# Kernel tuning notes

Measured on AMD Instinct MI355X. Metric: run time of the kernel, lower is better.

Reference implementation:

```python
import jax, jax.numpy as jnp
import numpy as np

B, L, S, V = 1024, 512, 64, 160000
EMB = 16
E = 3 * EMB            # extended embedding dim = 48
G, M = 4, 3            # lsh_group_num, lsh_group_length
MAXC = 2 ** M          # 8 buckets per group
NH, KD = 8, 4          # MHA heads / key_dim
IN_DIM = 5 * EMB + 3 * E   # user(80) + item(48) + longterm(48) + shortterm(48) = 224
PAD_LT, PAD_ST = L // 4, S // 4
M_VALUES = jnp.array([1, 2, 4], dtype=jnp.float32)
LN_EPS = 1e-3  # keras LayerNormalization default


def setup_inputs() -> dict:
    key = jax.random.key(0)
    ks = list(jax.random.split(key, 40))
    d = {}
    for i, n in enumerate(['uid', 'utag1', 'utag2', 'utag3', 'utag4']):
        d[n] = jax.random.randint(ks[i], (B,), 1, V, dtype=jnp.int32)
    for i, n in enumerate(['label_goods_ids', 'label_shop_ids', 'label_cate_ids']):
        d[n] = jax.random.randint(ks[5 + i], (B,), 1, V, dtype=jnp.int32)
    for i, n in enumerate(['longterm_goods_ids', 'longterm_shop_ids', 'longterm_cate_ids']):
        ids = jax.random.randint(ks[8 + i], (B, L), 1, V, dtype=jnp.int32)
        d[n] = ids.at[:, L - PAD_LT:].set(0)  # left-aligned valid prefix, padded tail
    for i, n in enumerate(['shortterm_goods_ids', 'shortterm_shop_ids', 'shortterm_cate_ids']):
        ids = jax.random.randint(ks[11 + i], (B, S), 1, V, dtype=jnp.int32)
        d[n] = ids.at[:, S - PAD_ST:].set(0)
    def nrm(k, shape, s):
        return jax.random.normal(k, shape, jnp.float32) * s
    d['embed_table'] = nrm(ks[14], (V, EMB), 0.05)
    d['H'] = nrm(ks[15], (E, G, M), 1.0)  # non-trainable LSH projections
    d['wq'] = nrm(ks[16], (E, NH, KD), 0.1); d['bq'] = jnp.zeros((NH, KD))
    d['wk'] = nrm(ks[17], (E, NH, KD), 0.1); d['bk'] = jnp.zeros((NH, KD))
    d['wv'] = nrm(ks[18], (E, NH, KD), 0.1); d['bv'] = jnp.zeros((NH, KD))
    d['wo'] = nrm(ks[19], (NH, KD, E), 0.1); d['bo'] = jnp.zeros((E,))
    d['w1'] = nrm(ks[20], (IN_DIM, 200), 0.1); d['b1'] = jnp.zeros((200,))
    d['g1'] = jnp.ones((200,)); d['be1'] = jnp.zeros((200,))
    d['w2'] = nrm(ks[21], (200, 80), 0.1); d['b2'] = jnp.zeros((80,))
    d['g2'] = jnp.ones((80,)); d['be2'] = jnp.zeros((80,))
    d['w3'] = nrm(ks[22], (80, 1), 0.1); d['b3'] = jnp.zeros((1,))
    return d


def _stack_embed(table, feats):
    # feats: list of (B,) or (B,T) int arrays -> (B, T, n_feats*EMB)
    cols = [f[:, None] if f.ndim == 1 else f for f in feats]
    X = jnp.stack(cols, axis=2)              # (B, T, F)
    Xe = table[X]                            # (B, T, F, EMB)
    return Xe.reshape(Xe.shape[0], Xe.shape[1], -1)


def _layernorm(x, g, b):
    mu = x.mean(-1, keepdims=True)
    var = jnp.square(x - mu).mean(-1, keepdims=True)
    return g * (x - mu) / jnp.sqrt(var + LN_EPS) + b


def _lsh_codes(x, H):
    # x: (B, T, E) -> integer bucket codes (B, T, G)
    codes = jnp.sign(jnp.einsum('bte,egm->btgm', x, H))
    binary = (codes == 1).astype(jnp.float32)
    return jnp.tensordot(binary, M_VALUES, axes=[[-1], [0]]).astype(jnp.int32)


def _forward(uid, utag1, utag2, utag3, utag4,
             label_goods_ids, label_shop_ids, label_cate_ids,
             longterm_goods_ids, longterm_shop_ids, longterm_cate_ids,
             shortterm_goods_ids, shortterm_shop_ids, shortterm_cate_ids,
             embed_table, H, wq, bq, wk, bk, wv, bv, wo, bo,
             w1, b1, g1, be1, w2, b2, g2, be2, w3, b3):
    # --- embeddings ---
    Xu = _stack_embed(embed_table, [uid, utag1, utag2, utag3, utag4])        # (B,1,80)
    Xi = _stack_embed(embed_table, [label_goods_ids, label_shop_ids, label_cate_ids])  # (B,1,48)
    Xl = _stack_embed(embed_table, [longterm_goods_ids, longterm_shop_ids, longterm_cate_ids])   # (B,L,48)
    Xs = _stack_embed(embed_table, [shortterm_goods_ids, shortterm_shop_ids, shortterm_cate_ids])  # (B,S,48)

    longterm_pad = longterm_goods_ids == 0
    shortterm_pad = shortterm_goods_ids == 0

    # --- long-term interest: LSH scatter-mean over buckets then gather by item code ---
    series_int = _lsh_codes(Xl, H)                                   # (B,L,G)
    mXl = Xl * (~longterm_pad).astype(jnp.float32)[:, :, None]        # masked series embeddings
    oh = jax.nn.one_hot(series_int, MAXC, dtype=jnp.float32)          # (B,L,G,C)
    c_sum = jnp.einsum('blgc,ble->bgce', oh, mXl)                     # bucket sums (B,G,C,E)
    vc = oh.sum(axis=1)                                               # valid counts (B,G,C)
    safe = jnp.where(vc[..., None] > 0,
                     c_sum / jnp.maximum(vc[..., None], 1.0),
                     0.0)                                             # bucket means
    item_int = _lsh_codes(Xi, H)                                      # (B,1,G)
    item_oh = jax.nn.one_hot(item_int, MAXC, dtype=jnp.float32)       # (B,1,G,C)
    longterm_interest = jnp.einsum('bgce,bsgc->bsge', safe, item_oh).mean(axis=2)  # (B,1,E)

    # --- short-term interest: target attention (keras MultiHeadAttention) ---
    lengths = (~shortterm_pad).astype(jnp.int32).sum(axis=1)           # (B,)
    seq_mask = (jnp.arange(S)[None, :] < lengths[:, None]).astype(jnp.float32)  # (B,S)
    q = jnp.einsum('bqe,ehd->bqhd', Xi, wq) + bq
    k = jnp.einsum('bke,ehd->bkhd', Xs, wk) + bk
    v = jnp.einsum('bke,ehd->bkhd', Xs, wv) + bv
    scores = jnp.einsum('bqhd,bkhd->bhqk', q, k) / jnp.sqrt(jnp.float32(KD))
    scores = scores + (1.0 - seq_mask[:, None, None, :]) * (-1e9)
    attn = jax.nn.softmax(scores, axis=-1)
    ctx = jnp.einsum('bhqk,bkhd->bqhd', attn, v)
    shortterm_interest = jnp.einsum('bqhd,hde->bqe', ctx, wo) + bo      # (B,1,E)

    # --- final MLP: Dense->LN->ReLU x2, Dense->sigmoid ---
    feat = jnp.concatenate([Xu[:, 0], Xi[:, 0],
                            longterm_interest[:, 0], shortterm_interest[:, 0]], axis=-1)  # (B,224)
    h = jax.nn.relu(_layernorm(feat @ w1 + b1, g1, be1))
    h = jax.nn.relu(_layernorm(h @ w2 + b2, g2, be2))
    return jax.nn.sigmoid(h @ w3 + b3)                                 # (B,1)


def reference(uid, utag1, utag2, utag3, utag4,
              label_goods_ids, label_shop_ids, label_cate_ids,
              longterm_goods_ids, longterm_shop_ids, longterm_cate_ids,
              shortterm_goods_ids, shortterm_shop_ids, shortterm_cate_ids,
              embed_table, H, wq, bq, wk, bk, wv, bv, wo, bo,
              w1, b1, g1, be1, w2, b2, g2, be2, w3, b3):
    return _forward(uid, utag1, utag2, utag3, utag4,
                    label_goods_ids, label_shop_ids, label_cate_ids,
                    longterm_goods_ids, longterm_shop_ids, longterm_cate_ids,
                    shortterm_goods_ids, shortterm_shop_ids, shortterm_cate_ids,
                    embed_table, H, wq, bq, wk, bk, wv, bv, wo, bo,
                    w1, b1, g1, be1, w2, b2, g2, be2, w3, b3)
```

## Files before the change

### kernel.cpp

```cpp
#include <hip/hip_runtime.h>
#include <hip/hip_bf16.h>

#define LLEN 512
#define SLEN 64
#define EMBD 16
#define EE 48
#define GG 4
#define NHH 8
#define KDD 4
#define INDIM 224
#define H1D 200
#define H2D 80
#define CHUNK 128
#define PXE 52
#define NT 512

__device__ __forceinline__ float bf2f(unsigned short u) {
    union { unsigned int i; float f; } v; v.i = ((unsigned int)u) << 16; return v.f;
}

template<bool BF16>
__device__ __forceinline__ float ldf(const void* p, int i) {
    if constexpr (BF16) return bf2f(((const unsigned short*)p)[i]);
    else                return ((const float*)p)[i];
}

template<bool BF16>
__device__ __forceinline__ float4 ld4(const void* p, int i4) {
    if constexpr (BF16) {
        ushort4 u = ((const ushort4*)p)[i4 >> 2];
        return make_float4(bf2f(u.x), bf2f(u.y), bf2f(u.z), bf2f(u.w));
    } else {
        return ((const float4*)p)[i4 >> 2];
    }
}

struct Pool {
    float buf[CHUNK * PXE + 16];
    float part[8][GG][EE];
    float hf[12 * EE];
    float feat[INDIM];
    float q[NHH * KDD];
    float red[128];
    int   pcw[8][2];
    int   len;
    float mu, rstd;
};

template<bool BF16>
__device__ void sdim_body(Pool& P,
    const int* uid, const int* ut1, const int* ut2, const int* ut3, const int* ut4,
    const int* lb_g, const int* lb_s, const int* lb_c,
    const int* lt_g, const int* lt_s, const int* lt_c,
    const int* st_g, const int* st_s, const int* st_c,
    const void* tbl, const void* Hm,
    const void* wq, const void* bq, const void* wk, const void* bk,
    const void* wvv, const void* bv, const void* wo, const void* bo,
    const void* w1, const void* b1, const void* g1, const void* be1,
    const void* w2, const void* b2, const void* g2, const void* be2,
    const void* w3, const void* b3, void* outp)
{
    const int b = blockIdx.x;
    const int tid = threadIdx.x;
    const int lane = tid & 63;
    const int wid = __builtin_amdgcn_readfirstlane(tid >> 6);

    const int pB = ((wid & 3) << 5) | (lane & 31);
    const int gB = ((wid >> 2) << 1) | (lane >> 5);

    int pid0, pid1, pid2, vld;
    {
        int f0 = tid, f1 = tid + NT, f2 = tid + 2 * NT;
        int p0 = f0 / 12, q0 = f0 - 12 * p0, e0 = q0 >> 2;
        int p1 = f1 / 12, q1 = f1 - 12 * p1, e1 = q1 >> 2;
        int p2 = f2 / 12, q2 = f2 - 12 * p2, e2 = q2 >> 2;
        const int* s0 = (e0 == 0) ? lt_g : (e0 == 1) ? lt_s : lt_c;
        const int* s1 = (e1 == 0) ? lt_g : (e1 == 1) ? lt_s : lt_c;
        const int* s2 = (e2 == 0) ? lt_g : (e2 == 1) ? lt_s : lt_c;
        pid0 = s0[b * LLEN + p0];
        pid1 = s1[b * LLEN + p1];
        pid2 = s2[b * LLEN + p2];
        vld  = lt_g[b * LLEN + pB];
    }

    for (int i = tid; i < 12 * EE; i += NT) {
        int j = i / EE, e = i - j * EE;
        P.hf[i] = ldf<BF16>(Hm, e * 12 + j);
    }
    if (tid < 80) {
        int f = tid >> 4, e = tid & 15;
        int id = (f == 0) ? uid[b] : (f == 1) ? ut1[b] : (f == 2) ? ut2[b] : (f == 3) ? ut3[b] : ut4[b];
        P.feat[tid] = ldf<BF16>(tbl, id * EMBD + e);
    } else if (tid < 128) {
        int t = tid - 80; int f = t >> 4, e = t & 15;
        int id = (f == 0) ? lb_g[b] : (f == 1) ? lb_s[b] : lb_c[b];
        P.feat[80 + t] = ldf<BF16>(tbl, id * EMBD + e);
    }
    __syncthreads();

    if (tid < 32) {
        float acc = ldf<BF16>(bq, tid);
        for (int e = 0; e < EE; e++) acc += P.feat[80 + e] * ldf<BF16>(wq, e * 32 + tid);
        P.q[tid] = acc;
    }
    if (tid >= 64 && tid < 76) {
        int j = tid - 64;
        float acc = 0.f;
        for (int e = 0; e < EE; e++) acc += P.feat[80 + e] * P.hf[j * EE + e];
        P.red[j] = acc;
    }
    __syncthreads();

    int icb = 0;
    #pragma unroll
    for (int m = 0; m < 3; m++) if (P.red[gB * 3 + m] > 0.f) icb |= (1 << m);

    float accg[GG] = {0.f, 0.f, 0.f, 0.f};
    int cnt0 = 0, cnt1 = 0;
    const int offs = (lane < 52) ? lane : 51;

    for (int ch = 0; ch < 4; ++ch) {
        {
            float4 v0, v1, v2;
            {
                int f0 = tid, f1 = tid + NT, f2 = tid + 2 * NT;
                int q0 = f0 - 12 * (f0 / 12);
                int q1 = f1 - 12 * (f1 / 12);
                int q2 = f2 - 12 * (f2 / 12);
                v0 = ld4<BF16>(tbl, pid0 * EMBD + ((q0 & 3) << 2));
                v1 = ld4<BF16>(tbl, pid1 * EMBD + ((q1 & 3) << 2));
                v2 = ld4<BF16>(tbl, pid2 * EMBD + ((q2 & 3) << 2));
            }
            {
                int f0 = tid, f1 = tid + NT, f2 = tid + 2 * NT;
                int p0 = f0 / 12, q0 = f0 - 12 * p0;
                int p1 = f1 / 12, q1 = f1 - 12 * p1;
                int p2 = f2 / 12, q2 = f2 - 12 * p2;
                *(float4*)&P.buf[p0 * PXE + (q0 << 2)] = v0;
                *(float4*)&P.buf[p1 * PXE + (q1 << 2)] = v1;
                *(float4*)&P.buf[p2 * PXE + (q2 << 2)] = v2;
            }
        }
        {
            const int nbase = ((ch < 3) ? (ch + 1) : 3) * CHUNK;
            int f0 = tid, f1 = tid + NT, f2 = tid + 2 * NT;
            int p0 = f0 / 12, e0 = (f0 - 12 * p0) >> 2;
            int p1 = f1 / 12, e1 = (f1 - 12 * p1) >> 2;
            int p2 = f2 / 12, e2 = (f2 - 12 * p2) >> 2;
            const int* s0 = (e0 == 0) ? lt_g : (e0 == 1) ? lt_s : lt_c;
            const int* s1 = (e1 == 0) ? lt_g : (e1 == 1) ? lt_s : lt_c;
            const int* s2 = (e2 == 0) ? lt_g : (e2 == 1) ? lt_s : lt_c;
            pid0 = s0[b * LLEN + nbase + p0];
            pid1 = s1[b * LLEN + nbase + p1];
            pid2 = s2[b * LLEN + nbase + p2];
        }
        __syncthreads();
        int nvld;
        {
            const int nbase = ((ch < 3) ? (ch + 1) : 3) * CHUNK;
            nvld = lt_g[b * LLEN + nbase + pB];
            const float* row = &P.buf[pB * PXE];
            float4 x[12];
            #pragma unroll
            for (int k = 0; k < 12; k++) x[k] = *(const float4*)(row + 4 * k);
            float acc[3];
            #pragma unroll
            for (int jj = 0; jj < 3; jj++) {
                const float4* hr = (const float4*)&P.hf[(3 * gB + jj) * EE];
                float s = 0.f;
                #pragma unroll
                for (int k = 0; k < 12; k++) {
                    float4 h4 = hr[k];
                    s += x[k].x * h4.x + x[k].y * h4.y + x[k].z * h4.z + x[k].w * h4.w;
                }
                acc[jj] = s;
            }
            int code = 0;
            #pragma unroll
            for (int m = 0; m < 3; m++) if (acc[m] > 0.f) code |= (1 << m);
            int valid = (vld != 0);
            P.buf[pB * PXE + 48 + gB] = (code == icb && valid) ? 1.f : 0.f;
            unsigned long long m = __ballot(code == icb);
            cnt0 += __popcll(m & 0xFFFFFFFFull);
            cnt1 += __popcll(m >> 32);
        }
        vld = nvld;
        __syncthreads();
        {
            const float* basep = &P.buf[(wid << 4) * PXE] + offs;
            #pragma unroll
            for (int i = 0; i < 16; i++) {
                float xv = basep[i * PXE];
                #pragma unroll
                for (int g = 0; g < GG; g++) {
                    float sel = __int_as_float(
                        __builtin_amdgcn_readlane(__float_as_int(xv), 48 + g));
                    accg[g] += sel * xv;
                }
            }
        }
        __syncthreads();
    }

    float* Xs   = P.buf;
    float* wkqT = P.buf + SLEN * PXE;
    float* bkq  = wkqT + NHH * PXE;
    float* sc   = bkq + NHH;
    float* su   = sc + SLEN * NHH;
    float* sctx = su + NHH * EE;

    if (lane < EE) {
        #pragma unroll
        for (int g = 0; g < GG; g++) P.part[wid][g][lane] = accg[g];
    }
    if (lane == 0) { P.pcw[wid][0] = cnt0; P.pcw[wid][1] = cnt1; }
    {
        int f0 = tid;
        int p0 = f0 / 12, q0 = f0 - 12 * p0, fe0 = q0 >> 2;
        const int* idp0 = (fe0 == 0) ? st_g : (fe0 == 1) ? st_s : st_c;
        int id0 = idp0[b * SLEN + p0];
        const bool has1 = (tid < (SLEN * 12 - NT));
        int id1 = 0, p1 = 0, q1 = 0;
        if (has1) {
            int f1 = tid + NT;
            p1 = f1 / 12; q1 = f1 - 12 * p1; int fe1 = q1 >> 2;
            const int* idp1 = (fe1 == 0) ? st_g : (fe1 == 1) ? st_s : st_c;
            id1 = idp1[b * SLEN + p1];
        }
        float4 v0 = ld4<BF16>(tbl, id0 * EMBD + ((q0 & 3) << 2));
        *(float4*)&Xs[p0 * PXE + (q0 << 2)] = v0;
        if (has1) {
            float4 v1 = ld4<BF16>(tbl, id1 * EMBD + ((q1 & 3) << 2));
            *(float4*)&Xs[p1 * PXE + (q1 << 2)] = v1;
        }
    }
    for (int t = tid; t < EE * NHH; t += NT) {
        int e = t >> 3, h = t & 7;
        float acc = 0.f;
        #pragma unroll
        for (int d = 0; d < KDD; d++) acc += ldf<BF16>(wk, e * 32 + h * 4 + d) * P.q[h * 4 + d];
        wkqT[h * PXE + e] = acc;
    }
    if (tid < NHH) {
        float acc = 0.f;
        #pragma unroll
        for (int d = 0; d < KDD; d++) acc += ldf<BF16>(bk, tid * 4 + d) * P.q[tid * 4 + d];
        bkq[tid] = acc;
    }
    if (tid < 64) {
        unsigned long long msk = __ballot(st_g[b * SLEN + tid] != 0);
        if (tid == 0) P.len = __popcll(msk);
    }
    __syncthreads();

    if (tid < EE) {
        float r = 0.f;
        #pragma unroll
        for (int g = 0; g < GG; g++) {
            int wb = (g >> 1) << 2;
            int h = g & 1;
            float c = (float)(P.pcw[wb][h] + P.pcw[wb + 1][h] + P.pcw[wb + 2][h] + P.pcw[wb + 3][h]);
            float s = 0.f;
            #pragma unroll
            for (int w = 0; w < 8; w++) s += P.part[w][g][tid];
            r += s / fmaxf(c, 1.0f);
        }
        P.feat[128 + tid] = r * 0.25f;
    }

    {
        int s = tid >> 3, h = tid & 7;
        const float* xr = &Xs[s * PXE];
        const float* wr = &wkqT[h * PXE];
        float acc = bkq[h];
        #pragma unroll
        for (int k = 0; k < 12; k++) {
            float4 xv = *(const float4*)(xr + 4 * k);
            float4 wv = *(const float4*)(wr + 4 * k);
            acc += xv.x * wv.x + xv.y * wv.y + xv.z * wv.z + xv.w * wv.w;
        }
        acc *= 0.5f;
        if (s >= P.len) acc -= 1e9f;
        sc[s * NHH + h] = acc;
    }
    __syncthreads();
    {
        float v = sc[lane * NHH + wid];
        float mx = v;
        #pragma unroll
        for (int o = 32; o; o >>= 1) mx = fmaxf(mx, __shfl_xor(mx, o));
        float ex = __expf(v - mx);
        float sm = ex;
        #pragma unroll
        for (int o = 32; o; o >>= 1) sm += __shfl_xor(sm, o);
        sc[lane * NHH + wid] = ex / sm;
    }
    __syncthreads();
    if (tid < NHH * EE) {
        int h = tid / EE, e = tid - h * EE;
        float acc = 0.f;
        #pragma unroll 4
        for (int s = 0; s < SLEN; s++) acc += sc[s * NHH + h] * Xs[s * PXE + e];
        su[tid] = acc;
    }
    __syncthreads();
    if (tid < 32) {
        float acc = ldf<BF16>(bv, tid);
        int h = tid >> 2;
        for (int e = 0; e < EE; e++) acc += su[h * EE + e] * ldf<BF16>(wvv, e * 32 + tid);
        sctx[tid] = acc;
    }
    __syncthreads();
    if (tid < EE) {
        float acc = ldf<BF16>(bo, tid);
        #pragma unroll
        for (int i = 0; i < 32; i++) acc += sctx[i] * ldf<BF16>(wo, i * EE + tid);
        P.feat[176 + tid] = acc;
    }
    __syncthreads();

    float z1p = 0.f;
    if (tid < H1D) {
        float a0 = ldf<BF16>(b1, tid), a1 = 0.f, a2 = 0.f, a3 = 0.f;
        #pragma unroll 2
        for (int i = 0; i < 112; i += 4) {
            float4 f4 = *(const float4*)&P.feat[i];
            a0 += f4.x * ldf<BF16>(w1, (i + 0) * H1D + tid);
            a1 += f4.y * ldf<BF16>(w1, (i + 1) * H1D + tid);
            a2 += f4.z * ldf<BF16>(w1, (i + 2) * H1D + tid);
            a3 += f4.w * ldf<BF16>(w1, (i + 3) * H1D + tid);
        }
        z1p = (a0 + a1) + (a2 + a3);
    } else if (tid >= 256 && tid < 256 + H1D) {
        int o = tid - 256;
        float a0 = 0.f, a1 = 0.f, a2 = 0.f, a3 = 0.f;
        #pragma unroll 2
        for (int i = 112; i < INDIM; i += 4) {
            float4 f4 = *(const float4*)&P.feat[i];
            a0 += f4.x * ldf<BF16>(w1, (i + 0) * H1D + o);
            a1 += f4.y * ldf<BF16>(w1, (i + 1) * H1D + o);
            a2 += f4.z * ldf<BF16>(w1, (i + 2) * H1D + o);
            a3 += f4.w * ldf<BF16>(w1, (i + 3) * H1D + o);
        }
        P.buf[640 + o] = (a0 + a1) + (a2 + a3);
    }
    __syncthreads();
    float z1 = 0.f;
    if (tid < H1D) { z1 = z1p + P.buf[640 + tid]; P.buf[tid] = z1; }
    __syncthreads();
    if (tid < 64) {
        float sm = 0.f, sq = 0.f;
        for (int j = tid; j < H1D; j += 64) { float v = P.buf[j]; sm += v; sq += v * v; }
        #pragma unroll
        for (int o = 32; o; o >>= 1) { sm += __shfl_xor(sm, o); sq += __shfl_xor(sq, o); }
        if (tid == 0) { float mu = sm / H1D; P.mu = mu; P.rstd = rsqrtf(sq / H1D - mu * mu + 1e-3f); }
    }
    __syncthreads();
    if (tid < H1D) {
        float h = fmaxf(ldf<BF16>(g1, tid) * (z1 - P.mu) * P.rstd + ldf<BF16>(be1, tid), 0.f);
        P.buf[256 + tid] = h;
    }
    __syncthreads();
    float z2p = 0.f;
    if (tid < H2D) {
        float a0 = ldf<BF16>(b2, tid), a1 = 0.f, a2 = 0.f, a3 = 0.f;
        #pragma unroll 2
        for (int i = 0; i < 100; i += 4) {
            float4 f4 = *(const float4*)&P.buf[256 + i];
            a0 += f4.x * ldf<BF16>(w2, (i + 0) * H2D + tid);
            a1 += f4.y * ldf<BF16>(w2, (i + 1) * H2D + tid);
            a2 += f4.z * ldf<BF16>(w2, (i + 2) * H2D + tid);
            a3 += f4.w * ldf<BF16>(w2, (i + 3) * H2D + tid);
        }
        z2p = (a0 + a1) + (a2 + a3);
    } else if (tid >= 256 && tid < 256 + H2D) {
        int o = tid - 256;
        float a0 = 0.f, a1 = 0.f, a2 = 0.f, a3 = 0.f;
        #pragma unroll 2
        for (int i = 100; i < H1D; i += 4) {
            float4 f4 = *(const float4*)&P.buf[256 + i];
            a0 += f4.x * ldf<BF16>(w2, (i + 0) * H2D + o);
            a1 += f4.y * ldf<BF16>(w2, (i + 1) * H2D + o);
            a2 += f4.z * ldf<BF16>(w2, (i + 2) * H2D + o);
            a3 += f4.w * ldf<BF16>(w2, (i + 3) * H2D + o);
        }
        P.buf[640 + o] = (a0 + a1) + (a2 + a3);
    }
    __syncthreads();
    float z2 = 0.f;
    if (tid < H2D) { z2 = z2p + P.buf[640 + tid]; P.buf[tid] = z2; }
    __syncthreads();
    if (tid < 64) {
        float sm = 0.f, sq = 0.f;
        for (int j = tid; j < H2D; j += 64) { float v = P.buf[j]; sm += v; sq += v * v; }
        #pragma unroll
        for (int o = 32; o; o >>= 1) { sm += __shfl_xor(sm, o); sq += __shfl_xor(sq, o); }
        if (tid == 0) { float mu = sm / H2D; P.mu = mu; P.rstd = rsqrtf(sq / H2D - mu * mu + 1e-3f); }
    }
    __syncthreads();
    if (tid < H2D) {
        float h = fmaxf(ldf<BF16>(g2, tid) * (z2 - P.mu) * P.rstd + ldf<BF16>(be2, tid), 0.f);
        P.red[tid] = h * ldf<BF16>(w3, tid);
    }
    __syncthreads();
    if (tid < 64) {
        float v = P.red[tid] + ((tid < H2D - 64) ? P.red[64 + tid] : 0.f);
        #pragma unroll
        for (int o = 32; o; o >>= 1) v += __shfl_xor(v, o);
        if (tid == 0) {
            float acc = ldf<BF16>(b3, 0) + v;
            float sig = 1.f / (1.f + __expf(-acc));
            if constexpr (BF16) ((__hip_bfloat16*)outp)[b] = __float2bfloat16(sig);
            else                ((float*)outp)[b] = sig;
        }
    }
}

__global__ __launch_bounds__(NT, 8) void sdim_fwd(
    const int* __restrict__ uid, const int* __restrict__ ut1, const int* __restrict__ ut2,
    const int* __restrict__ ut3, const int* __restrict__ ut4,
    const int* __restrict__ lb_g, const int* __restrict__ lb_s, const int* __restrict__ lb_c,
    const int* __restrict__ lt_g, const int* __restrict__ lt_s, const int* __restrict__ lt_c,
    const int* __restrict__ st_g, const int* __restrict__ st_s, const int* __restrict__ st_c,
    const void* __restrict__ tbl, const void* __restrict__ Hm,
    const void* __restrict__ wq, const void* __restrict__ bq,
    const void* __restrict__ wk, const void* __restrict__ bk,
    const void* __restrict__ wvv, const void* __restrict__ bv,
    const void* __restrict__ wo, const void* __restrict__ bo,
    const void* __restrict__ w1, const void* __restrict__ b1,
    const void* __restrict__ g1, const void* __restrict__ be1,
    const void* __restrict__ w2, const void* __restrict__ b2,
    const void* __restrict__ g2, const void* __restrict__ be2,
    const void* __restrict__ w3, const void* __restrict__ b3,
    void* __restrict__ outp)
{
    __shared__ Pool P;
    __shared__ int s_isbf;
    if (threadIdx.x < 64) {
        int big = 0;
        for (int i = (threadIdx.x & 63); i < 128; i += 64) {
            unsigned short u = ((const unsigned short*)tbl)[2 * i];
            if (((u >> 7) & 0xFF) >= 127) big = 1;
        }
        unsigned long long m = __ballot(big);
        if (threadIdx.x == 0) s_isbf = (m == 0ull) ? 1 : 0;
    }
    __syncthreads();
    if (s_isbf)
        sdim_body<true >(P, uid, ut1, ut2, ut3, ut4, lb_g, lb_s, lb_c, lt_g, lt_s, lt_c,
                         st_g, st_s, st_c, tbl, Hm, wq, bq, wk, bk, wvv, bv, wo, bo,
                         w1, b1, g1, be1, w2, b2, g2, be2, w3, b3, outp);
    else
        sdim_body<false>(P, uid, ut1, ut2, ut3, ut4, lb_g, lb_s, lb_c, lt_g, lt_s, lt_c,
                         st_g, st_s, st_c, tbl, Hm, wq, bq, wk, bk, wvv, bv, wo, bo,
                         w1, b1, g1, be1, w2, b2, g2, be2, w3, b3, outp);
}

extern "C" void kernel_launch(void* const* d_in, const int* in_sizes, int n_in,
                              void* d_out, int out_size, void* d_ws, size_t ws_size,
                              hipStream_t stream) {
    const int B = in_sizes[0];
    sdim_fwd<<<B, NT, 0, stream>>>(
        (const int*)d_in[0],  (const int*)d_in[1],  (const int*)d_in[2],
        (const int*)d_in[3],  (const int*)d_in[4],
        (const int*)d_in[5],  (const int*)d_in[6],  (const int*)d_in[7],
        (const int*)d_in[8],  (const int*)d_in[9],  (const int*)d_in[10],
        (const int*)d_in[11], (const int*)d_in[12], (const int*)d_in[13],
        (const void*)d_in[14], (const void*)d_in[15],
        (const void*)d_in[16], (const void*)d_in[17],
        (const void*)d_in[18], (const void*)d_in[19],
        (const void*)d_in[20], (const void*)d_in[21],
        (const void*)d_in[22], (const void*)d_in[23],
        (const void*)d_in[24], (const void*)d_in[25],
        (const void*)d_in[26], (const void*)d_in[27],
        (const void*)d_in[28], (const void*)d_in[29],
        (const void*)d_in[30], (const void*)d_in[31],
        (const void*)d_in[32], (const void*)d_in[33],
        d_out);
}
```

Measured before the change: 210.1 us.

## Stage all sequence ids in LDS up front and read selection flags from LDS

All long-term ids (3×512) are loaded once per block into LDS, reusing the `part` scratch area, and all short-term ids into a new `stids` array. This replaces the per-chunk prefetch of next-chunk ids and validity flags from global memory, so each chunk's table gather depends only on LDS reads. The grouped accumulation now reads the four bucket-match flags as one float4 from LDS instead of four cross-lane `readlane` ops. The short-term gathers are reordered so both table loads are issued before the stores. The cost is more up-front global traffic before the first barrier and losing the overlap the old id prefetch gave.

Result: slower. 233.9 us (+11.4%).

```diff
diff --git a/kernel.cpp b/kernel.cpp
--- a/kernel.cpp
+++ b/kernel.cpp
@@ -42,6 +42,7 @@
     float feat[INDIM];
     float q[NHH * KDD];
     float red[128];
+    int   stids[3 * SLEN];
     int   pcw[8][2];
     int   len;
     float mu, rstd;
@@ -68,21 +69,20 @@
     const int pB = ((wid & 3) << 5) | (lane & 31);
     const int gB = ((wid >> 2) << 1) | (lane >> 5);
 
-    int pid0, pid1, pid2, vld;
-    {
-        int f0 = tid, f1 = tid + NT, f2 = tid + 2 * NT;
-        int p0 = f0 / 12, q0 = f0 - 12 * p0, e0 = q0 >> 2;
-        int p1 = f1 / 12, q1 = f1 - 12 * p1, e1 = q1 >> 2;
-        int p2 = f2 / 12, q2 = f2 - 12 * p2, e2 = q2 >> 2;
-        const int* s0 = (e0 == 0) ? lt_g : (e0 == 1) ? lt_s : lt_c;
-        const int* s1 = (e1 == 0) ? lt_g : (e1 == 1) ? lt_s : lt_c;
-        const int* s2 = (e2 == 0) ? lt_g : (e2 == 1) ? lt_s : lt_c;
-        pid0 = s0[b * LLEN + p0];
-        pid1 = s1[b * LLEN + p1];
-        pid2 = s2[b * LLEN + p2];
-        vld  = lt_g[b * LLEN + pB];
-    }
-
+    int* IDS = (int*)P.part;
+
+    #pragma unroll
+    for (int r = 0; r < 3; r++) {
+        int i = tid + r * NT;
+        int fe = i >> 9, pos = i & 511;
+        const int* src = (fe == 0) ? lt_g : (fe == 1) ? lt_s : lt_c;
+        IDS[i] = __builtin_nontemporal_load(&src[b * LLEN + pos]);
+    }
+    if (tid < 3 * SLEN) {
+        int fe = tid >> 6, pos = tid & 63;
+        const int* src = (fe == 0) ? st_g : (fe == 1) ? st_s : st_c;
+        P.stids[tid] = __builtin_nontemporal_load(&src[b * SLEN + pos]);
+    }
     for (int i = tid; i < 12 * EE; i += NT) {
         int j = i / EE, e = i - j * EE;
         P.hf[i] = ldf<BF16>(Hm, e * 12 + j);
@@ -120,45 +120,25 @@
     const int offs = (lane < 52) ? lane : 51;
 
     for (int ch = 0; ch < 4; ++ch) {
+        const int base = ch * CHUNK;
         {
-            float4 v0, v1, v2;
-            {
-                int f0 = tid, f1 = tid + NT, f2 = tid + 2 * NT;
-                int q0 = f0 - 12 * (f0 / 12);
-                int q1 = f1 - 12 * (f1 / 12);
-                int q2 = f2 - 12 * (f2 / 12);
-                v0 = ld4<BF16>(tbl, pid0 * EMBD + ((q0 & 3) << 2));
-                v1 = ld4<BF16>(tbl, pid1 * EMBD + ((q1 & 3) << 2));
-                v2 = ld4<BF16>(tbl, pid2 * EMBD + ((q2 & 3) << 2));
-            }
-            {
-                int f0 = tid, f1 = tid + NT, f2 = tid + 2 * NT;
-                int p0 = f0 / 12, q0 = f0 - 12 * p0;
-                int p1 = f1 / 12, q1 = f1 - 12 * p1;
-                int p2 = f2 / 12, q2 = f2 - 12 * p2;
-                *(float4*)&P.buf[p0 * PXE + (q0 << 2)] = v0;
-                *(float4*)&P.buf[p1 * PXE + (q1 << 2)] = v1;
-                *(float4*)&P.buf[p2 * PXE + (q2 << 2)] = v2;
-            }
-        }
+            int f0 = tid, f1 = tid + NT, f2 = tid + 2 * NT;
+            int p0 = f0 / 12, q0 = f0 - 12 * p0, e0 = q0 >> 2;
+            int p1 = f1 / 12, q1 = f1 - 12 * p1, e1 = q1 >> 2;
+            int p2 = f2 / 12, q2 = f2 - 12 * p2, e2 = q2 >> 2;
+            int id0 = IDS[e0 * LLEN + base + p0];
+            int id1 = IDS[e1 * LLEN + base + p1];
+            int id2 = IDS[e2 * LLEN + base + p2];
+            float4 v0 = ld4<BF16>(tbl, id0 * EMBD + ((q0 & 3) << 2));
+            float4 v1 = ld4<BF16>(tbl, id1 * EMBD + ((q1 & 3) << 2));
+            float4 v2 = ld4<BF16>(tbl, id2 * EMBD + ((q2 & 3) << 2));
+            *(float4*)&P.buf[p0 * PXE + (q0 << 2)] = v0;
+            *(float4*)&P.buf[p1 * PXE + (q1 << 2)] = v1;
+            *(float4*)&P.buf[p2 * PXE + (q2 << 2)] = v2;
+        }
+        __syncthreads();
         {
-            const int nbase = ((ch < 3) ? (ch + 1) : 3) * CHUNK;
-            int f0 = tid, f1 = tid + NT, f2 = tid + 2 * NT;
-            int p0 = f0 / 12, e0 = (f0 - 12 * p0) >> 2;
-            int p1 = f1 / 12, e1 = (f1 - 12 * p1) >> 2;
-            int p2 = f2 / 12, e2 = (f2 - 12 * p2) >> 2;
-            const int* s0 = (e0 == 0) ? lt_g : (e0 == 1) ? lt_s : lt_c;
-            const int* s1 = (e1 == 0) ? lt_g : (e1 == 1) ? lt_s : lt_c;
-            const int* s2 = (e2 == 0) ? lt_g : (e2 == 1) ? lt_s : lt_c;
-            pid0 = s0[b * LLEN + nbase + p0];
-            pid1 = s1[b * LLEN + nbase + p1];
-            pid2 = s2[b * LLEN + nbase + p2];
-        }
-        __syncthreads();
-        int nvld;
-        {
-            const int nbase = ((ch < 3) ? (ch + 1) : 3) * CHUNK;
-            nvld = lt_g[b * LLEN + nbase + pB];
+            int valid = (IDS[base + pB] != 0);
             const float* row = &P.buf[pB * PXE];
             float4 x[12];
             #pragma unroll
@@ -178,25 +158,22 @@
             int code = 0;
             #pragma unroll
             for (int m = 0; m < 3; m++) if (acc[m] > 0.f) code |= (1 << m);
-            int valid = (vld != 0);
             P.buf[pB * PXE + 48 + gB] = (code == icb && valid) ? 1.f : 0.f;
             unsigned long long m = __ballot(code == icb);
             cnt0 += __popcll(m & 0xFFFFFFFFull);
             cnt1 += __popcll(m >> 32);
         }
-        vld = nvld;
         __syncthreads();
         {
-            const float* basep = &P.buf[(wid << 4) * PXE] + offs;
+            const float* basep = &P.buf[(wid << 4) * PXE];
             #pragma unroll
             for (int i = 0; i < 16; i++) {
-                float xv = basep[i * PXE];
-                #pragma unroll
-                for (int g = 0; g < GG; g++) {
-                    float sel = __int_as_float(
-                        __builtin_amdgcn_readlane(__float_as_int(xv), 48 + g));
-                    accg[g] += sel * xv;
-                }
+                float xv = basep[i * PXE + offs];
+                float4 sel = *(const float4*)(basep + i * PXE + 48);
+                accg[0] += sel.x * xv;
+                accg[1] += sel.y * xv;
+                accg[2] += sel.z * xv;
+                accg[3] += sel.w * xv;
             }
         }
         __syncthreads();
@@ -209,31 +186,28 @@
     float* su   = sc + SLEN * NHH;
     float* sctx = su + NHH * EE;
 
-    if (lane < EE) {
-        #pragma unroll
-        for (int g = 0; g < GG; g++) P.part[wid][g][lane] = accg[g];
-    }
-    if (lane == 0) { P.pcw[wid][0] = cnt0; P.pcw[wid][1] = cnt1; }
     {
         int f0 = tid;
         int p0 = f0 / 12, q0 = f0 - 12 * p0, fe0 = q0 >> 2;
-        const int* idp0 = (fe0 == 0) ? st_g : (fe0 == 1) ? st_s : st_c;
-        int id0 = idp0[b * SLEN + p0];
+        int id0 = P.stids[fe0 * SLEN + p0];
         const bool has1 = (tid < (SLEN * 12 - NT));
         int id1 = 0, p1 = 0, q1 = 0;
         if (has1) {
             int f1 = tid + NT;
             p1 = f1 / 12; q1 = f1 - 12 * p1; int fe1 = q1 >> 2;
-            const int* idp1 = (fe1 == 0) ? st_g : (fe1 == 1) ? st_s : st_c;
-            id1 = idp1[b * SLEN + p1];
+            id1 = P.stids[fe1 * SLEN + p1];
         }
         float4 v0 = ld4<BF16>(tbl, id0 * EMBD + ((q0 & 3) << 2));
+        float4 v1;
+        if (has1) v1 = ld4<BF16>(tbl, id1 * EMBD + ((q1 & 3) << 2));
         *(float4*)&Xs[p0 * PXE + (q0 << 2)] = v0;
-        if (has1) {
-            float4 v1 = ld4<BF16>(tbl, id1 * EMBD + ((q1 & 3) << 2));
-            *(float4*)&Xs[p1 * PXE + (q1 << 2)] = v1;
-        }
-    }
+        if (has1) *(float4*)&Xs[p1 * PXE + (q1 << 2)] = v1;
+    }
+    if (lane < EE) {
+        #pragma unroll
+        for (int g = 0; g < GG; g++) P.part[wid][g][lane] = accg[g];
+    }
+    if (lane == 0) { P.pcw[wid][0] = cnt0; P.pcw[wid][1] = cnt1; }
     for (int t = tid; t < EE * NHH; t += NT) {
         int e = t >> 3, h = t & 7;
         float acc = 0.f;
@@ -248,7 +222,7 @@
         bkq[tid] = acc;
     }
     if (tid < 64) {
-        unsigned long long msk = __ballot(st_g[b * SLEN + tid] != 0);
+        unsigned long long msk = __ballot(P.stids[tid] != 0);
         if (tid == 0) P.len = __popcll(msk);
     }
     __syncthreads();
```
